# Performance work log

Measured on AMD Instinct MI355X. Metric: run time of the kernel, lower is better.

Reference implementation:

```python
import jax, jax.numpy as jnp
import numpy as np

B, C, H, W = 32, 128, 64, 64
D = 256          # attn_unit_dim
FF = 512         # ffn latent dim (2.0 * 256, rounded to /16*16)
NL = 2           # n_attn_blocks
PH = PW = 2      # patch size
EPS = 1e-5


def _cf_ln(x, g, b):
    # channel-first LayerNorm over dim 1 (unbiased=False variance)
    m = jnp.mean(x, axis=1, keepdims=True)
    v = jnp.mean((x - m) ** 2, axis=1, keepdims=True)
    return (x - m) * jax.lax.rsqrt(v + EPS) * g.reshape(1, -1, 1, 1) + b.reshape(1, -1, 1, 1)


def _conv1x1(x, w, b=None):
    y = jnp.einsum('bcpq,dc->bdpq', x, w)
    return y if b is None else y + b.reshape(1, -1, 1, 1)


def _bn(x, g, b, m, v):
    # eval-mode BatchNorm2d with running stats
    return (x - m.reshape(1, -1, 1, 1)) * jax.lax.rsqrt(v.reshape(1, -1, 1, 1) + EPS) \
        * g.reshape(1, -1, 1, 1) + b.reshape(1, -1, 1, 1)


def setup_inputs() -> dict:
    key = jax.random.key(0)
    ks = iter(jax.random.split(key, 64))
    rn = lambda shape, s=0.02: jax.random.normal(next(ks), shape, jnp.float32) * s
    pv = lambda shape: 1.0 + 0.1 * jax.random.uniform(next(ks), shape, jnp.float32)
    return {
        'x': jax.random.normal(next(ks), (B, C, H, W), jnp.float32),
        # local_rep: depthwise 3x3 + BN + leaky_relu, then 1x1 -> D
        'dw_w': rn((C, 1, 3, 3), 0.1),
        'bn1_g': pv((C,)), 'bn1_b': rn((C,), 0.1),
        'bn1_m': rn((C,), 0.1), 'bn1_v': pv((C,)),
        'c1_w': rn((D, C)), 'c1_b': rn((D,), 0.01),
        # per-layer transformer params (stacked over NL)
        'ln1_g': pv((NL, D)), 'ln1_b': rn((NL, D), 0.1),
        'qkv_w': rn((NL, 1 + 2 * D, D)), 'qkv_b': rn((NL, 1 + 2 * D), 0.01),
        'out_w': rn((NL, D, D)), 'out_b': rn((NL, D), 0.01),
        'ln2_g': pv((NL, D)), 'ln2_b': rn((NL, D), 0.1),
        'f1_w': rn((NL, FF, D)), 'f1_b': rn((NL, FF), 0.01),
        'f2_w': rn((NL, D, FF)), 'f2_b': rn((NL, D), 0.01),
        'lnf_g': pv((D,)), 'lnf_b': rn((D,), 0.1),
        # conv_proj: 1x1 (no bias) + BN
        'proj_w': rn((C, D)),
        'bn2_g': pv((C,)), 'bn2_b': rn((C,), 0.1),
        'bn2_m': rn((C,), 0.1), 'bn2_v': pv((C,)),
    }


def reference(x, dw_w, bn1_g, bn1_b, bn1_m, bn1_v, c1_w, c1_b,
              ln1_g, ln1_b, qkv_w, qkv_b, out_w, out_b,
              ln2_g, ln2_b, f1_w, f1_b, f2_w, f2_b,
              lnf_g, lnf_b, proj_w, bn2_g, bn2_b, bn2_m, bn2_v):
    # local representation: depthwise 3x3 conv + BN + leaky_relu(0.1) + 1x1 conv
    y = jax.lax.conv_general_dilated(
        x, dw_w, window_strides=(1, 1), padding=[(1, 1), (1, 1)],
        dimension_numbers=('NCHW', 'OIHW', 'NCHW'), feature_group_count=C)
    y = _bn(y, bn1_g, bn1_b, bn1_m, bn1_v)
    y = jax.nn.leaky_relu(y, 0.1)
    y = _conv1x1(y, c1_w, c1_b)                       # [B, D, H, W]

    # unfold -> [B, D, P, N], P = PH*PW pixels/patch, N = patches
    nh, nw = H // PH, W // PW
    p = y.reshape(B, D, nh, PH, nw, PW).transpose(0, 1, 3, 5, 2, 4).reshape(B, D, PH * PW, nh * nw)

    # global representation: NL pre-norm linear-attention transformer blocks
    for l in range(NL):
        z = _cf_ln(p, ln1_g[l], ln1_b[l])
        qkv = _conv1x1(z, qkv_w[l], qkv_b[l])          # [B, 1+2D, P, N]
        q, k, v = qkv[:, :1], qkv[:, 1:1 + D], qkv[:, 1 + D:]
        scores = jax.nn.softmax(q, axis=-1)            # softmax over patches N
        ctx = jnp.sum(k * scores, axis=-1, keepdims=True)  # [B, D, P, 1]
        attn = _conv1x1(jax.nn.relu(v) * ctx, out_w[l], out_b[l])
        p = p + attn
        z = _cf_ln(p, ln2_g[l], ln2_b[l])
        h = jax.nn.leaky_relu(_conv1x1(z, f1_w[l], f1_b[l]), 0.1)
        p = p + _conv1x1(h, f2_w[l], f2_b[l])
    p = _cf_ln(p, lnf_g, lnf_b)

    # fold back -> [B, D, H, W]
    fm = p.reshape(B, D, PH, PW, nh, nw).transpose(0, 1, 4, 2, 5, 3).reshape(B, D, H, W)

    # conv_proj: 1x1 (no bias) + BN -> [B, C, H, W]
    fm = _conv1x1(fm, proj_w)
    fm = _bn(fm, bn2_g, bn2_b, bn2_m, bn2_v)
    return fm
```

## Files before the change

### kernel.cpp

```cpp
#include <hip/hip_runtime.h>


typedef short  bh8 __attribute__((ext_vector_type(8)));
typedef float  f4  __attribute__((ext_vector_type(4)));
typedef unsigned short us2 __attribute__((ext_vector_type(2)));
typedef unsigned short us4 __attribute__((ext_vector_type(4)));

constexpr int Bc = 32, Cc = 128, Dc = 256, FFc = 512;
constexpr int NNc = 1024, Sc = 4096;
constexpr float EPSc = 1e-5f;

enum SrcMode { S_LNF32, S_BF16 };
enum OutMode { O_STOREF32, O_FOLDBN };

__device__ __forceinline__ unsigned short f2bf(float f) {
  union { float f; unsigned int u; } v; v.f = f;
  unsigned int u = v.u + 0x7FFFu + ((v.u >> 16) & 1u);
  return (unsigned short)(u >> 16);
}

__global__ __launch_bounds__(256) void k_wconv(
    const float* __restrict__ w, unsigned short* __restrict__ dst,
    int total, int klog2)
{
  int idx = blockIdx.x * 256 + threadIdx.x;
  if (idx >= total) return;
  int K = 1 << klog2;
  int m = idx >> klog2, k = idx & (K - 1);
  int Mt = total >> klog2;
  size_t a = ((size_t)((k >> 5) * (Mt >> 4) + (m >> 4)) * 64
              + (((k >> 3) & 3) << 4) + (m & 15)) * 8 + (k & 7);
  dst[a] = f2bf(w[idx]);
}

__global__ __launch_bounds__(256) void k_dwconv(
    const float* __restrict__ x, const float* __restrict__ dww,
    const float* __restrict__ g, const float* __restrict__ bb,
    const float* __restrict__ mm, const float* __restrict__ vv,
    unsigned short* __restrict__ y1)
{
  int idx = blockIdx.x * 256 + threadIdx.x;
  int w4 = (idx & 15) * 4;
  int h  = (idx >> 4) & 63;
  int c  = (idx >> 10) & 127;
  int bi = idx >> 17;
  const float* xb = x + (size_t)(bi * 128 + c) * Sc;
  const float* wp = dww + c * 9;
  float acc[4] = {0.f, 0.f, 0.f, 0.f};
  #pragma unroll
  for (int kh = 0; kh < 3; ++kh) {
    int rr = h + kh - 1;
    if (rr < 0 || rr > 63) continue;
    const float* row = xb + rr * 64;
    float4 m4 = *reinterpret_cast<const float4*>(row + w4);
    float v[6];
    v[0] = (w4 > 0)  ? row[w4 - 1] : 0.f;
    v[1] = m4.x; v[2] = m4.y; v[3] = m4.z; v[4] = m4.w;
    v[5] = (w4 < 60) ? row[w4 + 4] : 0.f;
    float w0 = wp[kh * 3], w1 = wp[kh * 3 + 1], w2 = wp[kh * 3 + 2];
    #pragma unroll
    for (int o = 0; o < 4; ++o)
      acc[o] += w0 * v[o] + w1 * v[o + 1] + w2 * v[o + 2];
  }
  float sc = g[c] * rsqrtf(vv[c] + EPSc);
  float sh = bb[c] - mm[c] * sc;
  unsigned short r[4];
  #pragma unroll
  for (int o = 0; o < 4; ++o) {
    float val = acc[o] * sc + sh;
    r[o] = f2bf(val > 0.f ? val : 0.1f * val);
  }
  int ph = h & 1;
  size_t base = (size_t)(bi * 128 + c) * Sc + (h >> 1) * 32 + (w4 >> 1);
  *reinterpret_cast<us2*>(y1 + base + (ph * 2 + 0) * NNc) = (us2){r[0], r[2]};
  *reinterpret_cast<us2*>(y1 + base + (ph * 2 + 1) * NNc) = (us2){r[1], r[3]};
}

template<bool QD>
__global__ __launch_bounds__(256) void k_lnstats(
    const float* __restrict__ p, const float* __restrict__ wgq,
    float* __restrict__ mean_, float* __restrict__ rstd_, float* __restrict__ qdot)
{
  __shared__ float wg_s[256];
  int t = threadIdx.x;
  if (QD) { wg_s[t] = wgq[t]; __syncthreads(); }
  int pos = blockIdx.x * 256 + t;
  int b = pos >> 12, s = pos & 4095;
  const float* base = p + (size_t)b * Dc * Sc + s;
  float sum = 0.f, sq = 0.f, qa = 0.f;
  for (int d = 0; d < Dc; ++d) {
    float v = base[(size_t)d * Sc];
    sum += v; sq += v * v;
    if (QD) qa += v * wg_s[d];
  }
  float m   = sum * (1.f / Dc);
  float var = sq * (1.f / Dc) - m * m;
  mean_[pos] = m;
  rstd_[pos] = rsqrtf(fmaxf(var, 0.f) + EPSc);
  if (QD) qdot[pos] = qa;
}

__global__ void k_prep(const float* __restrict__ wq, const float* __restrict__ lng,
                       const float* __restrict__ lnb, const float* __restrict__ qb,
                       float* __restrict__ wgq, float* __restrict__ scal)
{
  int t = threadIdx.x, lane = t & 63, wv = t >> 6;
  float w = wq[t];
  float a = w * lng[t], c2 = w * lnb[t];
  wgq[t] = a;
  __shared__ float ra[4], rb[4];
  #pragma unroll
  for (int off = 32; off > 0; off >>= 1) { a += __shfl_xor(a, off); c2 += __shfl_xor(c2, off); }
  if (lane == 0) { ra[wv] = a; rb[wv] = c2; }
  __syncthreads();
  if (t == 0) {
    scal[0] = ra[0] + ra[1] + ra[2] + ra[3];
    scal[1] = rb[0] + rb[1] + rb[2] + rb[3] + qb[0];
  }
}

__global__ __launch_bounds__(256) void k_softmax2(
    const float* __restrict__ qdot, const float* __restrict__ mean_,
    const float* __restrict__ rstd_, const float* __restrict__ scal,
    float* __restrict__ ub, float* __restrict__ Ub)
{
  int bp = blockIdx.x, b = bp >> 2, pp = bp & 3;
  int t = threadIdx.x, lane = t & 63, wv = t >> 6;
  __shared__ float r3[4], r4[4];
  float s1 = scal[0], s2 = scal[1];
  int pos0 = b * Sc + pp * NNc;
  float q[4], m_r[4], rs_r[4];
  float mx = -3.4e38f;
  #pragma unroll
  for (int i = 0; i < 4; ++i) {
    int pos = pos0 + t + i * 256;
    m_r[i] = mean_[pos]; rs_r[i] = rstd_[pos];
    q[i] = rs_r[i] * qdot[pos] - m_r[i] * rs_r[i] * s1 + s2;
    mx = fmaxf(mx, q[i]);
  }
  #pragma unroll
  for (int off = 32; off > 0; off >>= 1) mx = fmaxf(mx, __shfl_xor(mx, off));
  if (lane == 0) r3[wv] = mx;
  __syncthreads();
  mx = fmaxf(fmaxf(r3[0], r3[1]), fmaxf(r3[2], r3[3]));
  float sum = 0.f;
  #pragma unroll
  for (int i = 0; i < 4; ++i) { q[i] = __expf(q[i] - mx); sum += q[i]; }
  #pragma unroll
  for (int off = 32; off > 0; off >>= 1) sum += __shfl_xor(sum, off);
  if (lane == 0) r4[wv] = sum;
  __syncthreads();
  float inv = 1.f / (r4[0] + r4[1] + r4[2] + r4[3]);
  float pU = 0.f;
  #pragma unroll
  for (int i = 0; i < 4; ++i) {
    float un = rs_r[i] * q[i] * inv;
    ub[(size_t)bp * NNc + t + i * 256] = un;
    pU += m_r[i] * un;
  }
  #pragma unroll
  for (int off = 32; off > 0; off >>= 1) pU += __shfl_xor(pU, off);
  if (lane == 0) r3[wv] = pU;
  __syncthreads();
  if (t == 0) Ub[bp] = r3[0] + r3[1] + r3[2] + r3[3];
}

__global__ __launch_bounds__(256) void k_tpass(
    const float* __restrict__ p, const float* __restrict__ ub,
    const float* __restrict__ Ub, const float* __restrict__ lng,
    const float* __restrict__ lnb, float* __restrict__ tb)
{
  int cs = blockIdx.x, pp = blockIdx.y, b = blockIdx.z;
  int bp = b * 4 + pp;
  int t = threadIdx.x, lane = t & 63, wv = t >> 6;
  __shared__ float u_s[1024];
  for (int i = t; i < 1024; i += 256) u_s[i] = ub[(size_t)bp * NNc + i];
  __syncthreads();
  float U = Ub[bp];
  const float* pb = p + (size_t)b * Dc * Sc + pp * NNc;
  for (int i = 0; i < 16; ++i) {
    int c = cs * 64 + wv * 16 + i;
    const float* row = pb + (size_t)c * Sc;
    float sm = 0.f;
    #pragma unroll
    for (int j = 0; j < 16; ++j) { int n = lane + 64 * j; sm += row[n] * u_s[n]; }
    #pragma unroll
    for (int off = 32; off > 0; off >>= 1) sm += __shfl_xor(sm, off);
    if (lane == 0) tb[(size_t)bp * Dc + c] = lng[c] * (sm - U) + lnb[c];
  }
}

__global__ __launch_bounds__(256) void k_ctx2(
    const float* __restrict__ tb, const float* __restrict__ wk,
    const float* __restrict__ bk, float* __restrict__ ctxb)
{
  int b = blockIdx.x, d = threadIdx.x;
  __shared__ float ts[4][256];
  for (int i = threadIdx.x; i < 1024; i += 256) ts[i >> 8][i & 255] = tb[(size_t)b * 1024 + i];
  __syncthreads();
  const float* wrow = wk + (size_t)d * 256;
  float bkd = bk[d];
  float accp[4] = {0.f, 0.f, 0.f, 0.f};
  for (int c = 0; c < 256; c += 4) {
    float4 wv = *reinterpret_cast<const float4*>(wrow + c);
    #pragma unroll
    for (int pp = 0; pp < 4; ++pp)
      accp[pp] += wv.x * ts[pp][c] + wv.y * ts[pp][c + 1]
                + wv.z * ts[pp][c + 2] + wv.w * ts[pp][c + 3];
  }
  #pragma unroll
  for (int pp = 0; pp < 4; ++pp)
    ctxb[((size_t)(b * 256 + d)) * 4 + pp] = accp[pp] + bkd;
}

__global__ void k_bn2pre(const float* __restrict__ g, const float* __restrict__ bb,
                         const float* __restrict__ mm, const float* __restrict__ vv,
                         float* __restrict__ sc, float* __restrict__ sh)
{
  int c = threadIdx.x;
  if (c < Cc) {
    float s = g[c] * rsqrtf(vv[c] + EPSc);
    sc[c] = s;
    sh[c] = bb[c] - mm[c] * s;
  }
}

template<int M1, bool ATTN>
__global__ __launch_bounds__(256) void k_fused(
    const float* __restrict__ p,
    const float* __restrict__ mean_, const float* __restrict__ rstd_,
    const float* __restrict__ lng, const float* __restrict__ lnb,
    const unsigned short* __restrict__ wf1, const float* __restrict__ b1,
    const float* __restrict__ ctxp,
    const unsigned short* __restrict__ wf2, const float* __restrict__ b2,
    float* __restrict__ dst)
{
  constexpr int NT = 32;
  constexpr int NF = NT / 16;
  constexpr int ACC1 = M1 / 64;
  int t = threadIdx.x;
  int wv = t >> 6, lane = t & 63;
  int q = lane >> 4, ln16 = lane & 15;
  int nt = blockIdx.x, pp = blockIdx.y, b = blockIdx.z;
  int n0 = nt * NT;

  __shared__ unsigned int Alds[2][NT * 20];
  __shared__ unsigned short Frag[M1 * NT];
  __shared__ float m_s[NT], rs_s[NT];
  __shared__ float ctx_s[ATTN ? 256 : 4];

  int kp_s = t >> 4;
  int n2_s = (t & 15) * 2;

  size_t pbase = (size_t)b * Dc * Sc + pp * NNc + n0;

  float2 c0 = *reinterpret_cast<const float2*>(p + pbase + (size_t)(kp_s * 2) * Sc + n2_s);
  float2 c1 = *reinterpret_cast<const float2*>(p + pbase + (size_t)(kp_s * 2 + 1) * Sc + n2_s);

  if (t < NT) {
    int pos = b * Sc + pp * NNc + n0 + t;
    m_s[t]  = mean_[pos];
    rs_s[t] = rstd_[pos];
  }
  if (ATTN) ctx_s[t] = ctxp[(size_t)(b * Dc + t) * 4 + pp];

  f4 acc[ACC1][NF];
  #pragma unroll
  for (int i = 0; i < ACC1; ++i)
    #pragma unroll
    for (int j = 0; j < NF; ++j) acc[i][j] = (f4){0.f, 0.f, 0.f, 0.f};

  __syncthreads();

  for (int kc = 0; kc < 256; kc += 32) {
    int k0 = kc + kp_s * 2;
    float g0 = lng[k0], g1 = lng[k0 + 1];
    float h0 = lnb[k0], h1 = lnb[k0 + 1];
    float ms0 = m_s[n2_s],     rs0 = rs_s[n2_s];
    float ms1 = m_s[n2_s + 1], rs1 = rs_s[n2_s + 1];
    float a00 = (c0.x - ms0) * rs0 * g0 + h0;
    float a01 = (c0.y - ms1) * rs1 * g0 + h0;
    float a10 = (c1.x - ms0) * rs0 * g1 + h1;
    float a11 = (c1.y - ms1) * rs1 * g1 + h1;
    unsigned int pk0 = (unsigned int)f2bf(a00) | ((unsigned int)f2bf(a10) << 16);
    unsigned int pk1 = (unsigned int)f2bf(a01) | ((unsigned int)f2bf(a11) << 16);

    if (kc < 224) {
      c0 = *reinterpret_cast<const float2*>(p + pbase + (size_t)(kc + 32 + kp_s * 2) * Sc + n2_s);
      c1 = *reinterpret_cast<const float2*>(p + pbase + (size_t)(kc + 32 + kp_s * 2 + 1) * Sc + n2_s);
    }

    unsigned int* alw = Alds[(kc >> 5) & 1];
    alw[n2_s * 20 + kp_s]       = pk0;
    alw[(n2_s + 1) * 20 + kp_s] = pk1;

    bh8 aw[ACC1];
    #pragma unroll
    for (int tm = 0; tm < ACC1; ++tm)
      aw[tm] = *(const bh8*)(wf1 + ((size_t)((kc >> 5) * (M1 >> 4) + wv * ACC1 + tm) * 64 + lane) * 8);

    __syncthreads();

    const unsigned short* al = (const unsigned short*)Alds[(kc >> 5) & 1];
    #pragma unroll
    for (int tn = 0; tn < NF; ++tn) {
      bh8 bwf = *(const bh8*)(al + (tn * 16 + ln16) * 40 + q * 8);
      #pragma unroll
      for (int tm = 0; tm < ACC1; ++tm)
        acc[tm][tn] = __builtin_amdgcn_mfma_f32_16x16x32_bf16(aw[tm], bwf, acc[tm][tn], 0, 0, 0);
    }
  }

  #pragma unroll
  for (int tm = 0; tm < ACC1; ++tm) {
    int row0 = wv * (M1 / 4) + tm * 16 + q * 4;
    float bia[4], cxv[4];
    #pragma unroll
    for (int r = 0; r < 4; ++r) {
      bia[r] = b1[row0 + r];
      if (ATTN) cxv[r] = ctx_s[row0 + r];
    }
    int kt  = row0 >> 5;
    int sub = (row0 >> 3) & 3;
    int jo  = row0 & 7;
    #pragma unroll
    for (int tn = 0; tn < NF; ++tn) {
      int cl = tn * 16 + ln16;
      us4 pk;
      #pragma unroll
      for (int r = 0; r < 4; ++r) {
        float v = acc[tm][tn][r] + bia[r];
        if (ATTN) v = fmaxf(v, 0.f) * cxv[r];
        else      v = v > 0.f ? v : 0.1f * v;
        pk[r] = f2bf(v);
      }
      *reinterpret_cast<us4*>(Frag + (((kt * NF + (cl >> 4)) * 64 + (sub << 4 | (cl & 15))) * 8 + jo)) = pk;
    }
  }
  __syncthreads();

  f4 acc2[4][NF];
  #pragma unroll
  for (int i = 0; i < 4; ++i)
    #pragma unroll
    for (int j = 0; j < NF; ++j) acc2[i][j] = (f4){0.f, 0.f, 0.f, 0.f};

  for (int kc = 0; kc < M1; kc += 32) {
    bh8 aw2[4];
    #pragma unroll
    for (int tm = 0; tm < 4; ++tm)
      aw2[tm] = *(const bh8*)(wf2 + ((size_t)((kc >> 5) * 16 + wv * 4 + tm) * 64 + lane) * 8);
    #pragma unroll
    for (int tn = 0; tn < NF; ++tn) {
      bh8 bwf = *(const bh8*)(Frag + ((kc >> 5) * NF + tn) * 512 + lane * 8);
      #pragma unroll
      for (int tm = 0; tm < 4; ++tm)
        acc2[tm][tn] = __builtin_amdgcn_mfma_f32_16x16x32_bf16(aw2[tm], bwf, acc2[tm][tn], 0, 0, 0);
    }
  }

  #pragma unroll
  for (int tm = 0; tm < 4; ++tm) {
    #pragma unroll
    for (int r = 0; r < 4; ++r) {
      int row = wv * 64 + tm * 16 + q * 4 + r;
      float bv = b2[row];
      #pragma unroll
      for (int tn = 0; tn < NF; ++tn) {
        int col = n0 + tn * 16 + ln16;
        size_t da = (size_t)(b * Dc + row) * Sc + pp * NNc + col;
        dst[da] += acc2[tm][tn][r] + bv;
      }
    }
  }
}

template<int KTOT, int MTOT, int SRCCH, int SSTR, bool SPP,
         SrcMode SM, OutMode OM>
__global__ __launch_bounds__(256) void k_mm(
    const void* __restrict__ src,
    const float* __restrict__ mean_, const float* __restrict__ rstd_,
    const float* __restrict__ lng, const float* __restrict__ lnb,
    const unsigned short* __restrict__ wf, const float* __restrict__ bias,
    const float* __restrict__ bnsc, const float* __restrict__ bnsh,
    void* __restrict__ dst)
{
  int t = threadIdx.x;
  int wv = t >> 6, lane = t & 63;
  int wm = wv & 1, wn = wv >> 1;
  int q = lane >> 4, ln16 = lane & 15;
  int nb = blockIdx.x, b = blockIdx.z;
  int pp = blockIdx.y & 3, mb = blockIdx.y >> 2;
  int n0  = nb * 128;
  int MB0 = mb * 128;

  __shared__ unsigned int Alds[128 * 20];
  __shared__ float m_s[128], rs_s[128];

  if (SM == S_LNF32 && t < 128) {
    int pos = b * Sc + pp * NNc + n0 + t;
    m_s[t]  = mean_[pos];
    rs_s[t] = rstd_[pos];
  }

  f4 acc[4][4];
  #pragma unroll
  for (int i = 0; i < 4; ++i)
    #pragma unroll
    for (int j = 0; j < 4; ++j) acc[i][j] = (f4){0.f, 0.f, 0.f, 0.f};

  size_t sbase = (size_t)b * SRCCH * SSTR + pp * NNc + n0;
  int mtb = (MB0 >> 4) + wm * 4;

  for (int kc = 0; kc < KTOT; kc += 32) {
    bh8 aw[4];
    #pragma unroll
    for (int tm = 0; tm < 4; ++tm)
      aw[tm] = *(const bh8*)(wf + ((size_t)((kc >> 5) * (MTOT >> 4) + mtb + tm) * 64 + lane) * 8);
    __syncthreads();
    #pragma unroll
    for (int it = 0; it < 8; ++it) {
      int n_l = (t & 63) + (it & 1) * 64;
      int kp  = (t >> 6) + (it >> 1) * 4;
      int k0  = kc + kp * 2;
      unsigned int pk;
      if (SM == S_LNF32) {
        const float* sp = (const float*)src;
        float a0 = sp[sbase + (size_t)k0 * SSTR + n_l];
        float a1 = sp[sbase + (size_t)(k0 + 1) * SSTR + n_l];
        float ms = m_s[n_l], rs = rs_s[n_l];
        a0 = (a0 - ms) * rs * lng[k0] + lnb[k0];
        a1 = (a1 - ms) * rs * lng[k0 + 1] + lnb[k0 + 1];
        pk = (unsigned int)f2bf(a0) | ((unsigned int)f2bf(a1) << 16);
      } else {
        const unsigned short* sp = (const unsigned short*)src;
        unsigned int u0 = sp[sbase + (size_t)k0 * SSTR + n_l];
        unsigned int u1 = sp[sbase + (size_t)(k0 + 1) * SSTR + n_l];
        pk = u0 | (u1 << 16);
      }
      Alds[n_l * 20 + kp] = pk;
    }
    __syncthreads();
    const unsigned short* al = (const unsigned short*)Alds;
    #pragma unroll
    for (int tn = 0; tn < 4; ++tn) {
      int nrow = wn * 64 + tn * 16 + ln16;
      bh8 bwf = *(const bh8*)(al + nrow * 40 + q * 8);
      #pragma unroll
      for (int tm = 0; tm < 4; ++tm)
        acc[tm][tn] = __builtin_amdgcn_mfma_f32_16x16x32_bf16(aw[tm], bwf, acc[tm][tn], 0, 0, 0);
    }
  }

  #pragma unroll
  for (int tm = 0; tm < 4; ++tm) {
    #pragma unroll
    for (int r = 0; r < 4; ++r) {
      int row = MB0 + wm * 64 + tm * 16 + q * 4 + r;
      float scv = 0.f, shv = 0.f, bv = 0.f;
      if (OM == O_FOLDBN) { scv = bnsc[row]; shv = bnsh[row]; }
      else                { bv = bias[row]; }
      #pragma unroll
      for (int tn = 0; tn < 4; ++tn) {
        int col = n0 + wn * 64 + tn * 16 + ln16;
        float v = acc[tm][tn][r];
        if (OM == O_FOLDBN) {
          int hh = 2 * (col >> 5) + (pp >> 1), ww = 2 * (col & 31) + (pp & 1);
          ((float*)dst)[((size_t)(b * Cc + row)) * Sc + hh * 64 + ww] = v * scv + shv;
        } else {
          ((float*)dst)[(size_t)(b * MTOT + row) * Sc + pp * NNc + col] = v + bv;
        }
      }
    }
  }
}

extern "C" void kernel_launch(void* const* d_in, const int* in_sizes, int n_in,
                              void* d_out, int out_size, void* d_ws, size_t ws_size,
                              hipStream_t stream)
{
  const float* x     = (const float*)d_in[0];
  const float* dw_w  = (const float*)d_in[1];
  const float* bn1_g = (const float*)d_in[2];
  const float* bn1_b = (const float*)d_in[3];
  const float* bn1_m = (const float*)d_in[4];
  const float* bn1_v = (const float*)d_in[5];
  const float* c1_w  = (const float*)d_in[6];
  const float* c1_b  = (const float*)d_in[7];
  const float* ln1_g = (const float*)d_in[8];
  const float* ln1_b = (const float*)d_in[9];
  const float* qkv_w = (const float*)d_in[10];
  const float* qkv_b = (const float*)d_in[11];
  const float* out_w = (const float*)d_in[12];
  const float* out_b = (const float*)d_in[13];
  const float* ln2_g = (const float*)d_in[14];
  const float* ln2_b = (const float*)d_in[15];
  const float* f1_w  = (const float*)d_in[16];
  const float* f1_b  = (const float*)d_in[17];
  const float* f2_w  = (const float*)d_in[18];
  const float* f2_b  = (const float*)d_in[19];
  const float* lnf_g = (const float*)d_in[20];
  const float* lnf_b = (const float*)d_in[21];
  const float* projw = (const float*)d_in[22];
  const float* bn2_g = (const float*)d_in[23];
  const float* bn2_b = (const float*)d_in[24];
  const float* bn2_m = (const float*)d_in[25];
  const float* bn2_v = (const float*)d_in[26];
  float* out = (float*)d_out;

  float* ws    = (float*)d_ws;
  float* p     = ws;
  float* reg   = p + (size_t)33554432;
  unsigned short* y1u = (unsigned short*)reg;
  float* meanb = reg   + (size_t)8388608;
  float* rstdb = meanb + 131072;
  float* qdotb = rstdb + 131072;
  float* ub    = qdotb + 131072;
  float* Ub    = ub    + 131072;
  float* tb    = Ub    + 128;
  float* ctxb  = tb    + 32768;
  float* wgq   = ctxb  + 32768;
  float* scal  = wgq   + 256;
  float* bnscb = scal  + 16;
  float* bnshb = bnscb + 128;
  unsigned short* wfb = (unsigned short*)(bnshb + 128);
  unsigned short* wf_c1   = wfb;
  unsigned short* wf_v0   = wfb + 32768;
  unsigned short* wf_proj = wfb + 32768 + 2 * 393216;

  k_wconv<<<128, 256, 0, stream>>>(c1_w, wf_c1, 256 * 128, 7);
  for (int l = 0; l < 2; ++l) {
    const float* wvp = qkv_w + ((size_t)l * 513 + 257) * Dc;
    unsigned short* base = wf_v0 + (size_t)l * 393216;
    k_wconv<<<256, 256, 0, stream>>>(wvp, base, 256 * 256, 8);
    k_wconv<<<256, 256, 0, stream>>>(out_w + (size_t)l * Dc * Dc, base + 65536, 256 * 256, 8);
    k_wconv<<<512, 256, 0, stream>>>(f1_w + (size_t)l * FFc * Dc, base + 131072, 512 * 256, 8);
    k_wconv<<<512, 256, 0, stream>>>(f2_w + (size_t)l * Dc * FFc, base + 262144, 256 * 512, 9);
  }
  k_wconv<<<128, 256, 0, stream>>>(projw, wf_proj, 128 * 256, 8);

  k_dwconv<<<16384, 256, 0, stream>>>(x, dw_w, bn1_g, bn1_b, bn1_m, bn1_v, y1u);

  k_mm<128, 256, 128, 4096, true, S_BF16, O_STOREF32>
      <<<dim3(8, 8, 32), 256, 0, stream>>>(
      y1u, nullptr, nullptr, nullptr, nullptr, wf_c1, c1_b, nullptr, nullptr, p);

  for (int l = 0; l < 2; ++l) {
    const float* g1 = ln1_g + l * Dc; const float* b1 = ln1_b + l * Dc;
    const float* g2 = ln2_g + l * Dc; const float* b2 = ln2_b + l * Dc;
    const float* wq = qkv_w + (size_t)l * 513 * Dc;
    const float* wk = qkv_w + ((size_t)l * 513 + 1) * Dc;
    const float* bq = qkv_b + l * 513;
    const float* bk = qkv_b + l * 513 + 1;
    const float* bvv = qkv_b + l * 513 + 257;
    unsigned short* wbase = wf_v0 + (size_t)l * 393216;

    k_prep<<<1, 256, 0, stream>>>(wq, g1, b1, bq, wgq, scal);
    k_lnstats<true><<<512, 256, 0, stream>>>(p, wgq, meanb, rstdb, qdotb);
    k_softmax2<<<128, 256, 0, stream>>>(qdotb, meanb, rstdb, scal, ub, Ub);
    k_tpass<<<dim3(4, 4, 32), 256, 0, stream>>>(p, ub, Ub, g1, b1, tb);
    k_ctx2<<<32, 256, 0, stream>>>(tb, wk, bk, ctxb);

    k_fused<256, true><<<dim3(32, 4, 32), 256, 0, stream>>>(
        p, meanb, rstdb, g1, b1, wbase, bvv, ctxb,
        wbase + 65536, out_b + l * Dc, p);

    k_lnstats<false><<<512, 256, 0, stream>>>(p, nullptr, meanb, rstdb, nullptr);
    k_fused<512, false><<<dim3(32, 4, 32), 256, 0, stream>>>(
        p, meanb, rstdb, g2, b2, wbase + 131072, f1_b + l * FFc, nullptr,
        wbase + 262144, f2_b + l * Dc, p);
  }

  k_lnstats<false><<<512, 256, 0, stream>>>(p, nullptr, meanb, rstdb, nullptr);
  k_bn2pre<<<1, 128, 0, stream>>>(bn2_g, bn2_b, bn2_m, bn2_v, bnscb, bnshb);
  k_mm<256, 128, 256, 4096, true, S_LNF32, O_FOLDBN>
      <<<dim3(8, 4, 32), 256, 0, stream>>>(
      p, meanb, rstdb, lnf_g, lnf_b, wf_proj, nullptr, bnscb, bnshb, out);
}
```

Before: 920.5 us.

## Fuse LayerNorm statistics and q-dot into fused block epilogues

```diff
diff --git a/kernel.cpp b/kernel.cpp
--- a/kernel.cpp
+++ b/kernel.cpp
@@ -225,7 +225,7 @@
   }
 }
 
-template<int M1, bool ATTN>
+template<int M1, bool ATTN, bool QDOT>
 __global__ __launch_bounds__(256) void k_fused(
     const float* __restrict__ p,
     const float* __restrict__ mean_, const float* __restrict__ rstd_,
@@ -233,7 +233,10 @@
     const unsigned short* __restrict__ wf1, const float* __restrict__ b1,
     const float* __restrict__ ctxp,
     const unsigned short* __restrict__ wf2, const float* __restrict__ b2,
-    float* __restrict__ dst)
+    float* __restrict__ dst,
+    const float* __restrict__ wgq2,
+    float* __restrict__ mean_o, float* __restrict__ rstd_o,
+    float* __restrict__ qdot_o)
 {
   constexpr int NT = 32;
   constexpr int NF = NT / 16;
@@ -359,19 +362,59 @@
     }
   }
 
+  float s1[NF], s2[NF], s3[NF];
+  #pragma unroll
+  for (int tn = 0; tn < NF; ++tn) { s1[tn] = 0.f; s2[tn] = 0.f; s3[tn] = 0.f; }
   #pragma unroll
   for (int tm = 0; tm < 4; ++tm) {
     #pragma unroll
     for (int r = 0; r < 4; ++r) {
       int row = wv * 64 + tm * 16 + q * 4 + r;
       float bv = b2[row];
+      float wqr = QDOT ? wgq2[row] : 0.f;
       #pragma unroll
       for (int tn = 0; tn < NF; ++tn) {
         int col = n0 + tn * 16 + ln16;
         size_t da = (size_t)(b * Dc + row) * Sc + pp * NNc + col;
-        dst[da] += acc2[tm][tn][r] + bv;
+        float v = dst[da] + acc2[tm][tn][r] + bv;
+        dst[da] = v;
+        s1[tn] += v; s2[tn] += v * v;
+        if (QDOT) s3[tn] += v * wqr;
       }
     }
+  }
+  #pragma unroll
+  for (int tn = 0; tn < NF; ++tn) {
+    s1[tn] += __shfl_xor(s1[tn], 16); s1[tn] += __shfl_xor(s1[tn], 32);
+    s2[tn] += __shfl_xor(s2[tn], 16); s2[tn] += __shfl_xor(s2[tn], 32);
+    if (QDOT) { s3[tn] += __shfl_xor(s3[tn], 16); s3[tn] += __shfl_xor(s3[tn], 32); }
+  }
+  __syncthreads();
+  float* fr = (float*)Frag;
+  if (q == 0) {
+    #pragma unroll
+    for (int tn = 0; tn < NF; ++tn) {
+      int col = tn * 16 + ln16;
+      fr[(wv * 3 + 0) * NT + col] = s1[tn];
+      fr[(wv * 3 + 1) * NT + col] = s2[tn];
+      fr[(wv * 3 + 2) * NT + col] = s3[tn];
+    }
+  }
+  __syncthreads();
+  if (t < NT) {
+    float a1 = 0.f, a2 = 0.f, a3 = 0.f;
+    #pragma unroll
+    for (int w2 = 0; w2 < 4; ++w2) {
+      a1 += fr[(w2 * 3 + 0) * NT + t];
+      a2 += fr[(w2 * 3 + 1) * NT + t];
+      a3 += fr[(w2 * 3 + 2) * NT + t];
+    }
+    int pos = b * Sc + pp * NNc + n0 + t;
+    float mn  = a1 * (1.f / 256.f);
+    float var = a2 * (1.f / 256.f) - mn * mn;
+    mean_o[pos] = mn;
+    rstd_o[pos] = rsqrtf(fmaxf(var, 0.f) + EPSc);
+    if (QDOT) qdot_o[pos] = a3;
   }
 }
 
@@ -512,6 +555,8 @@
   float* p     = ws;
   float* reg   = p + (size_t)33554432;
   unsigned short* y1u = (unsigned short*)reg;
+  float* mean2 = reg;
+  float* rstd2 = reg + 131072;
   float* meanb = reg   + (size_t)8388608;
   float* rstdb = meanb + 131072;
   float* qdotb = rstdb + 131072;
@@ -520,7 +565,7 @@
   float* tb    = Ub    + 128;
   float* ctxb  = tb    + 32768;
   float* wgq   = ctxb  + 32768;
-  float* scal  = wgq   + 256;
+  float* scal  = wgq   + 512;
   float* bnscb = scal  + 16;
   float* bnshb = bnscb + 128;
   unsigned short* wfb = (unsigned short*)(bnshb + 128);
@@ -539,39 +584,49 @@
   }
   k_wconv<<<128, 256, 0, stream>>>(projw, wf_proj, 128 * 256, 8);
 
+  for (int l = 0; l < 2; ++l)
+    k_prep<<<1, 256, 0, stream>>>(qkv_w + (size_t)l * 513 * Dc,
+                                  ln1_g + l * Dc, ln1_b + l * Dc,
+                                  qkv_b + l * 513, wgq + l * 256, scal + l * 2);
+
   k_dwconv<<<16384, 256, 0, stream>>>(x, dw_w, bn1_g, bn1_b, bn1_m, bn1_v, y1u);
 
   k_mm<128, 256, 128, 4096, true, S_BF16, O_STOREF32>
       <<<dim3(8, 8, 32), 256, 0, stream>>>(
       y1u, nullptr, nullptr, nullptr, nullptr, wf_c1, c1_b, nullptr, nullptr, p);
 
+  k_lnstats<true><<<512, 256, 0, stream>>>(p, wgq, meanb, rstdb, qdotb);
+
   for (int l = 0; l < 2; ++l) {
     const float* g1 = ln1_g + l * Dc; const float* b1 = ln1_b + l * Dc;
     const float* g2 = ln2_g + l * Dc; const float* b2 = ln2_b + l * Dc;
-    const float* wq = qkv_w + (size_t)l * 513 * Dc;
     const float* wk = qkv_w + ((size_t)l * 513 + 1) * Dc;
-    const float* bq = qkv_b + l * 513;
     const float* bk = qkv_b + l * 513 + 1;
     const float* bvv = qkv_b + l * 513 + 257;
     unsigned short* wbase = wf_v0 + (size_t)l * 393216;
 
-    k_prep<<<1, 256, 0, stream>>>(wq, g1, b1, bq, wgq, scal);
-    k_lnstats<true><<<512, 256, 0, stream>>>(p, wgq, meanb, rstdb, qdotb);
-    k_softmax2<<<128, 256, 0, stream>>>(qdotb, meanb, rstdb, scal, ub, Ub);
+    k_softmax2<<<128, 256, 0, stream>>>(qdotb, meanb, rstdb, scal + l * 2, ub, Ub);
     k_tpass<<<dim3(4, 4, 32), 256, 0, stream>>>(p, ub, Ub, g1, b1, tb);
     k_ctx2<<<32, 256, 0, stream>>>(tb, wk, bk, ctxb);
 
-    k_fused<256, true><<<dim3(32, 4, 32), 256, 0, stream>>>(
+    k_fused<256, true, false><<<dim3(32, 4, 32), 256, 0, stream>>>(
         p, meanb, rstdb, g1, b1, wbase, bvv, ctxb,
-        wbase + 65536, out_b + l * Dc, p);
-
-    k_lnstats<false><<<512, 256, 0, stream>>>(p, nullptr, meanb, rstdb, nullptr);
-    k_fused<512, false><<<dim3(32, 4, 32), 256, 0, stream>>>(
-        p, meanb, rstdb, g2, b2, wbase + 131072, f1_b + l * FFc, nullptr,
-        wbase + 262144, f2_b + l * Dc, p);
-  }
-
-  k_lnstats<false><<<512, 256, 0, stream>>>(p, nullptr, meanb, rstdb, nullptr);
+        wbase + 65536, out_b + l * Dc, p,
+        nullptr, mean2, rstd2, nullptr);
+
+    if (l == 0) {
+      k_fused<512, false, true><<<dim3(32, 4, 32), 256, 0, stream>>>(
+          p, mean2, rstd2, g2, b2, wbase + 131072, f1_b + l * FFc, nullptr,
+          wbase + 262144, f2_b + l * Dc, p,
+          wgq + 256, meanb, rstdb, qdotb);
+    } else {
+      k_fused<512, false, false><<<dim3(32, 4, 32), 256, 0, stream>>>(
+          p, mean2, rstd2, g2, b2, wbase + 131072, f1_b + l * FFc, nullptr,
+          wbase + 262144, f2_b + l * Dc, p,
+          nullptr, meanb, rstdb, nullptr);
+    }
+  }
+
   k_bn2pre<<<1, 128, 0, stream>>>(bn2_g, bn2_b, bn2_m, bn2_v, bnscb, bnshb);
   k_mm<256, 128, 256, 4096, true, S_LNF32, O_FOLDBN>
       <<<dim3(8, 4, 32), 256, 0, stream>>>(
```

Measured after the change: 780.0 us. -15.3%, faster.
